# Optimization experiments

Hardware: AMD Instinct MI355X
Metric: run time of the kernel (lower is better)

The kernel has to match this reference:

```python
import jax, jax.numpy as jnp
import numpy as np
from jax import lax

T, H, I, E, K = 1024, 1024, 512, 16, 4


def setup_inputs() -> dict:
    key = jax.random.key(0)
    k1, k2, k3, k4, k5 = jax.random.split(key, 5)
    hidden_states = jax.random.normal(k1, (T, H), dtype=jnp.float32)
    top_k_index = jax.random.randint(k2, (T, K), 0, E)
    top_k_weights = jax.random.uniform(k3, (T, K), dtype=jnp.float32)
    gate_up_proj = jax.random.normal(k4, (E, 2 * I, H), dtype=jnp.float32) * 0.02
    down_proj = jax.random.normal(k5, (E, H, I), dtype=jnp.float32) * 0.02
    return {
        "hidden_states": hidden_states,
        "top_k_index": top_k_index,
        "top_k_weights": top_k_weights,
        "gate_up_proj": gate_up_proj,
        "down_proj": down_proj,
    }


def reference(hidden_states, top_k_index, top_k_weights, gate_up_proj, down_proj):
    num_experts = gate_up_proj.shape[0]
    # combine[t, e] = sum_k top_k_weights[t, k] * [top_k_index[t, k] == e]
    # Expert output is linear in the routing weight, so summing weights over
    # duplicate (token, expert) hits matches the original index_add_ exactly.
    one_hot = jax.nn.one_hot(top_k_index, num_experts, dtype=hidden_states.dtype)  # [T, K, E]
    combine = jnp.einsum("tke,tk->te", one_hot, top_k_weights)  # [T, E]

    def expert_step(acc, xs):
        w_gu, w_d, c = xs  # [2I, H], [H, I], [T]
        gu = hidden_states @ w_gu.T          # [T, 2I]
        gate, up = jnp.split(gu, 2, axis=-1)
        h = jax.nn.silu(gate) * up            # [T, I]
        out = h @ w_d.T                       # [T, H]
        return acc + out * c[:, None], None

    final, _ = lax.scan(
        expert_step,
        jnp.zeros_like(hidden_states),
        (gate_up_proj, down_proj, combine.T),
    )
    return final
```

## Files before the change

kernel.cpp:

```cpp
#include <hip/hip_runtime.h>
#include <hip/hip_bf16.h>
#include <cstdint>
#include <cstddef>

#define T_TOK 1024
#define HDIM  1024
#define IDIM  512
#define NEXP  16
#define TOPK  4
#define CAP   1024

typedef __bf16 bf16;
typedef __attribute__((ext_vector_type(8))) __bf16 bf16x8;
typedef __attribute__((ext_vector_type(4))) __bf16 bf16x4;
typedef __attribute__((ext_vector_type(4))) float f32x4;

__device__ __forceinline__ void lds_load16(void* lds_dst, const void* g_src) {
  __builtin_amdgcn_global_load_lds(
      (__attribute__((address_space(1))) unsigned int*)(void*)(g_src),
      (__attribute__((address_space(3))) unsigned int*)(lds_dst),
      16, 0, 0);
}

__device__ __forceinline__ bf16x4 cvt4(float4 a) {
  bf16x4 o;
  o[0] = (bf16)a.x; o[1] = (bf16)a.y; o[2] = (bf16)a.z; o[3] = (bf16)a.w;
  return o;
}


#define CVT_BLOCKS (T_TOK * HDIM / 4 / 256)

__global__ void prep_kernel(const float* __restrict__ hid_f, bf16* __restrict__ hid_b,
                            const int* __restrict__ idx, const float* __restrict__ w,
                            int* __restrict__ etk, float* __restrict__ ew,
                            int* __restrict__ cntpad, float* __restrict__ out) {
  __shared__ int cnt;
  const int b = blockIdx.x;
  const int tid = threadIdx.x;
  if (b < CVT_BLOCKS) {
    int i = b * 256 + tid;
    float4 v = ((const float4*)hid_f)[i];
    ((bf16x4*)hid_b)[i] = cvt4(v);
    ((float4*)out)[i] = make_float4(0.f, 0.f, 0.f, 0.f);
    if (b == 0)
      ((bf16x4*)(hid_b + (size_t)T_TOK * HDIM))[tid] = cvt4(make_float4(0.f, 0.f, 0.f, 0.f));
    return;
  }
  const int e = b - CVT_BLOCKS;
  if (tid == 0) cnt = 0;
  __syncthreads();
  for (int j = tid; j < T_TOK * TOPK; j += blockDim.x) {
    if (idx[j] == e) {
      int slot = atomicAdd(&cnt, 1);
      if (slot < CAP) { etk[e * CAP + slot] = j; ew[e * CAP + slot] = w[j]; }
    }
  }
  __syncthreads();
  int c = cnt < CAP ? cnt : CAP;
  int p = (c + 127) & ~127;
  for (int j = c + tid; j < p; j += blockDim.x) {
    etk[e * CAP + j] = (T_TOK << 2);
    ew[e * CAP + j] = 0.f;
  }
  if (tid == 0) cntpad[e] = p;
}


__global__ __launch_bounds__(256, 4) void gemm1_kernel(
    const bf16* __restrict__ hid,
    const float* __restrict__ gup,
    const int* __restrict__ etk, const float* __restrict__ ew,
    const int* __restrict__ cntpad,
    bf16* __restrict__ hsc) {
  __shared__ __align__(16) bf16 As[2][128 * 64];
  __shared__ __align__(16) bf16 Bs[2][32 * 64];
  const int e = blockIdx.y;
  const int ntiles = cntpad[e] >> 7;
  const int n0 = blockIdx.x * 16;
  const int ebase = e * CAP;
  const int tid = threadIdx.x, lane = tid & 63, wid = tid >> 6;
  const int wm = wid * 32;
  const int lcol = lane & 15, lquad = lane >> 4;
  const int l7 = lcol & 7;
  const int srow = tid >> 3;
  const int swz = ((tid & 7) ^ (srow & 7)) * 8;
  const int r = tid >> 3;
  const int c0 = (tid & 7) * 8;
  const int grow = (r < 16) ? (n0 + r) : (IDIM + n0 + (r - 16));
  const float* gB = gup + (size_t)e * (2 * IDIM) * HDIM + (size_t)grow * HDIM + c0;
  int wb[2];
#pragma unroll
  for (int j = 0; j < 2; ++j) {
    int c = c0 + 4 * j;
    wb[j] = (((c >> 3) ^ (r & 7)) * 8) + (c & 7);
  }
  const int bst = r * 64;

  for (int mt = 0; mt < ntiles; ++mt) {
    const int mrow = ebase + mt * 128;
    const bf16* gA[4];
#pragma unroll
    for (int q = 0; q < 4; ++q)
      gA[q] = hid + (size_t)(etk[mrow + srow + 32 * q] >> 2) * HDIM + swz;
    f32x4 aG[2], aU[2];
#pragma unroll
    for (int mf = 0; mf < 2; ++mf) {
      aG[mf] = f32x4{0.f, 0.f, 0.f, 0.f};
      aU[mf] = f32x4{0.f, 0.f, 0.f, 0.f};
    }
    {
      float4 bv[2];
#pragma unroll
      for (int j = 0; j < 2; ++j) bv[j] = *(const float4*)(gB + 4 * j);
#pragma unroll
      for (int q = 0; q < 4; ++q)
        lds_load16(&As[0][tid * 8 + q * 2048], gA[q]);
#pragma unroll
      for (int j = 0; j < 2; ++j)
        *(bf16x4*)&Bs[0][bst + wb[j]] = cvt4(bv[j]);
    }
    __syncthreads();
#pragma unroll 2
    for (int k = 0; k < 16; ++k) {
      const int cur = k & 1, nxt = cur ^ 1;
      float4 bn[2];
      if (k < 15) {
#pragma unroll
        for (int q = 0; q < 4; ++q)
          lds_load16(&As[nxt][tid * 8 + q * 2048], gA[q] + (k + 1) * 64);
#pragma unroll
        for (int j = 0; j < 2; ++j)
          bn[j] = *(const float4*)(gB + (k + 1) * 64 + 4 * j);
      }
      __builtin_amdgcn_s_setprio(1);
#pragma unroll
      for (int ks = 0; ks < 2; ++ks) {
        const int lch = ks * 4 + lquad;
        const int sw = (lch ^ l7) * 8;
        bf16x8 bg = *(const bf16x8*)&Bs[cur][lcol * 64 + sw];
        bf16x8 bu = *(const bf16x8*)&Bs[cur][(16 + lcol) * 64 + sw];
#pragma unroll
        for (int mf = 0; mf < 2; ++mf) {
          bf16x8 af = *(const bf16x8*)&As[cur][(wm + mf * 16 + lcol) * 64 + sw];
          aG[mf] = __builtin_amdgcn_mfma_f32_16x16x32_bf16(af, bg, aG[mf], 0, 0, 0);
          aU[mf] = __builtin_amdgcn_mfma_f32_16x16x32_bf16(af, bu, aU[mf], 0, 0, 0);
        }
      }
      __builtin_amdgcn_s_setprio(0);
      if (k < 15) {
#pragma unroll
        for (int j = 0; j < 2; ++j)
          *(bf16x4*)&Bs[nxt][bst + wb[j]] = cvt4(bn[j]);
      }
      __syncthreads();
    }
#pragma unroll
    for (int mf = 0; mf < 2; ++mf) {
#pragma unroll
      for (int rr = 0; rr < 4; ++rr) {
        const int erow = mt * 128 + wm + mf * 16 + lquad * 4 + rr;
        const float wgt = ew[ebase + erow];
        float g = aG[mf][rr], u = aU[mf][rr];
        float s = g / (1.f + __expf(-g));
        hsc[(size_t)(ebase + erow) * IDIM + n0 + lcol] = (bf16)(s * u * wgt);
      }
    }
  }
}


__global__ __launch_bounds__(256, 4) void gemm2_kernel(
    const bf16* __restrict__ hsc,
    const float* __restrict__ down,
    const int* __restrict__ etk, const int* __restrict__ cntpad,
    float* __restrict__ out) {
  __shared__ __align__(16) bf16 As[2][128 * 64];
  __shared__ __align__(16) bf16 Bs[2][32 * 64];
  const int flat = blockIdx.y * 32 + blockIdx.x;
  const int wkid = (flat & 7) * 64 + (flat >> 3);
  const int e = wkid >> 5;
  const int n0 = (wkid & 31) * 32;
  const int ntiles = cntpad[e] >> 7;
  const int ebase = e * CAP;
  const int tid = threadIdx.x, lane = tid & 63, wid = tid >> 6;
  const int wm = wid * 32;
  const int lcol = lane & 15, lquad = lane >> 4;
  const int l7 = lcol & 7;
  const int srow = tid >> 3;
  const int swz = ((tid & 7) ^ (srow & 7)) * 8;
  const int r = tid >> 3;
  const int c0 = (tid & 7) * 8;
  const float* gB = down + (size_t)e * HDIM * IDIM + (size_t)(n0 + r) * IDIM + c0;
  int wb[2];
#pragma unroll
  for (int j = 0; j < 2; ++j) {
    int c = c0 + 4 * j;
    wb[j] = (((c >> 3) ^ (r & 7)) * 8) + (c & 7);
  }
  const int bst = r * 64;

  for (int mt = 0; mt < ntiles; ++mt) {
    const size_t rbase = (size_t)(ebase + mt * 128);
    const bf16* gA[4];
#pragma unroll
    for (int q = 0; q < 4; ++q)
      gA[q] = hsc + (rbase + srow + 32 * q) * IDIM + swz;
    f32x4 acc[2][2];
#pragma unroll
    for (int mf = 0; mf < 2; ++mf) {
      acc[mf][0] = f32x4{0.f, 0.f, 0.f, 0.f};
      acc[mf][1] = f32x4{0.f, 0.f, 0.f, 0.f};
    }
    {
      float4 bv[2];
#pragma unroll
      for (int j = 0; j < 2; ++j) bv[j] = *(const float4*)(gB + 4 * j);
#pragma unroll
      for (int q = 0; q < 4; ++q)
        lds_load16(&As[0][tid * 8 + q * 2048], gA[q]);
#pragma unroll
      for (int j = 0; j < 2; ++j)
        *(bf16x4*)&Bs[0][bst + wb[j]] = cvt4(bv[j]);
    }
    __syncthreads();
#pragma unroll 2
    for (int k = 0; k < 8; ++k) {
      const int cur = k & 1, nxt = cur ^ 1;
      float4 bn[2];
      if (k < 7) {
#pragma unroll
        for (int q = 0; q < 4; ++q)
          lds_load16(&As[nxt][tid * 8 + q * 2048], gA[q] + (k + 1) * 64);
#pragma unroll
        for (int j = 0; j < 2; ++j)
          bn[j] = *(const float4*)(gB + (k + 1) * 64 + 4 * j);
      }
      __builtin_amdgcn_s_setprio(1);
#pragma unroll
      for (int ks = 0; ks < 2; ++ks) {
        const int lch = ks * 4 + lquad;
        const int sw = (lch ^ l7) * 8;
        bf16x8 b0 = *(const bf16x8*)&Bs[cur][lcol * 64 + sw];
        bf16x8 b1 = *(const bf16x8*)&Bs[cur][(16 + lcol) * 64 + sw];
#pragma unroll
        for (int mf = 0; mf < 2; ++mf) {
          bf16x8 af = *(const bf16x8*)&As[cur][(wm + mf * 16 + lcol) * 64 + sw];
          acc[mf][0] = __builtin_amdgcn_mfma_f32_16x16x32_bf16(af, b0, acc[mf][0], 0, 0, 0);
          acc[mf][1] = __builtin_amdgcn_mfma_f32_16x16x32_bf16(af, b1, acc[mf][1], 0, 0, 0);
        }
      }
      __builtin_amdgcn_s_setprio(0);
      if (k < 7) {
#pragma unroll
        for (int j = 0; j < 2; ++j)
          *(bf16x4*)&Bs[nxt][bst + wb[j]] = cvt4(bn[j]);
      }
      __syncthreads();
    }
#pragma unroll
    for (int mf = 0; mf < 2; ++mf) {
#pragma unroll
      for (int rr = 0; rr < 4; ++rr) {
        const int row = mt * 128 + wm + mf * 16 + lquad * 4 + rr;
        const int tk = etk[ebase + row];
        const int tok = tk >> 2;
        if (tok < T_TOK) {
          float* orow = out + (size_t)tok * HDIM + n0 + lcol;
          atomicAdd(orow, acc[mf][0][rr]);
          atomicAdd(orow + 16, acc[mf][1][rr]);
        }
      }
    }
  }
}


extern "C" void kernel_launch(void* const* d_in, const int* in_sizes, int n_in,
                              void* d_out, int out_size, void* d_ws, size_t ws_size,
                              hipStream_t stream) {
  const float* hid_f  = (const float*)d_in[0];
  const int*   idx    = (const int*)d_in[1];
  const float* tw     = (const float*)d_in[2];
  const float* gup_f  = (const float*)d_in[3];
  const float* down_f = (const float*)d_in[4];
  float* out = (float*)d_out;

  uint8_t* ws = (uint8_t*)d_ws;
  size_t off = 0;
  bf16* hid_b = (bf16*)(ws + off);   off += (size_t)(T_TOK + 1) * HDIM * 2;
  int*  etk   = (int*)(ws + off);    off += (size_t)NEXP * CAP * 4;
  float* ewt  = (float*)(ws + off);  off += (size_t)NEXP * CAP * 4;
  int* cntpad = (int*)(ws + off);    off += 256;
  bf16* hsc   = (bf16*)(ws + off);

  prep_kernel<<<dim3(CVT_BLOCKS + NEXP), dim3(256), 0, stream>>>(
      hid_f, hid_b, idx, tw, etk, ewt, cntpad, out);
  gemm1_kernel<<<dim3(IDIM / 16, NEXP, 1), dim3(256), 0, stream>>>(
      hid_b, gup_f, etk, ewt, cntpad, hsc);
  gemm2_kernel<<<dim3(HDIM / 32, NEXP, 1), dim3(256), 0, stream>>>(
      hsc, down_f, etk, cntpad, out);
}
```

Before: 209.6 us.

## Flatten expert GEMMs into per-tile grids with 64-row tiles and per-wave B

Both GEMM kernels stop looping over an expert's row tiles inside one block. Instead they launch a flattened grid of (expert, 64-row tile) entries, with a lookup over the padded per-expert counts; padding granularity drops from 128 to 64. Each wave now converts and stages its own private fp32→bf16 weight slice in LDS, and the next slice is prefetched in registers. The goal is more blocks in flight and better load balance across uneven expert loads. The cost is redundant tile-lookup work, blocks that exit early beyond the real tile count, and a larger register footprint for the prefetch buffers.

```diff
diff --git a/kernel.cpp b/kernel.cpp
--- a/kernel.cpp
+++ b/kernel.cpp
@@ -9,11 +9,15 @@
 #define NEXP  16
 #define TOPK  4
 #define CAP   1024
+#define MAXTILES 80
 
 typedef __bf16 bf16;
 typedef __attribute__((ext_vector_type(8))) __bf16 bf16x8;
 typedef __attribute__((ext_vector_type(4))) __bf16 bf16x4;
 typedef __attribute__((ext_vector_type(4))) float f32x4;
+
+#define BAR() __builtin_amdgcn_s_barrier()
+#define SB()  __builtin_amdgcn_sched_barrier(0)
 
 __device__ __forceinline__ void lds_load16(void* lds_dst, const void* g_src) {
   __builtin_amdgcn_global_load_lds(
@@ -26,6 +30,17 @@
   bf16x4 o;
   o[0] = (bf16)a.x; o[1] = (bf16)a.y; o[2] = (bf16)a.z; o[3] = (bf16)a.w;
   return o;
+}
+
+__device__ __forceinline__ bool tile_lookup(const int* cntpad, int idx,
+                                            int& e_out, int& mt_out) {
+  int rem = idx;
+  for (int e = 0; e < NEXP; ++e) {
+    int nt = cntpad[e] >> 6;
+    if (rem < nt) { e_out = e; mt_out = rem; return true; }
+    rem -= nt;
+  }
+  return false;
 }
 
 
@@ -58,7 +73,7 @@
   }
   __syncthreads();
   int c = cnt < CAP ? cnt : CAP;
-  int p = (c + 127) & ~127;
+  int p = (c + 63) & ~63;
   for (int j = c + tid; j < p; j += blockDim.x) {
     etk[e * CAP + j] = (T_TOK << 2);
     ew[e * CAP + j] = 0.f;
@@ -73,98 +88,102 @@
     const int* __restrict__ etk, const float* __restrict__ ew,
     const int* __restrict__ cntpad,
     bf16* __restrict__ hsc) {
-  __shared__ __align__(16) bf16 As[2][128 * 64];
-  __shared__ __align__(16) bf16 Bs[2][32 * 64];
-  const int e = blockIdx.y;
-  const int ntiles = cntpad[e] >> 7;
-  const int n0 = blockIdx.x * 16;
+  __shared__ __align__(16) bf16 As[2][64 * 64];
+  __shared__ __align__(16) bf16 Bp[4][32 * 64];
+  int e, mt;
+  if (!tile_lookup(cntpad, blockIdx.y, e, mt)) return;
+  const int n0 = blockIdx.x * 32;
   const int ebase = e * CAP;
   const int tid = threadIdx.x, lane = tid & 63, wid = tid >> 6;
-  const int wm = wid * 32;
+  const int wm = (wid >> 1) * 32, wi = (wid & 1) * 16;
   const int lcol = lane & 15, lquad = lane >> 4;
   const int l7 = lcol & 7;
   const int srow = tid >> 3;
   const int swz = ((tid & 7) ^ (srow & 7)) * 8;
-  const int r = tid >> 3;
-  const int c0 = (tid & 7) * 8;
-  const int grow = (r < 16) ? (n0 + r) : (IDIM + n0 + (r - 16));
-  const float* gB = gup + (size_t)e * (2 * IDIM) * HDIM + (size_t)grow * HDIM + c0;
-  int wb[2];
-#pragma unroll
-  for (int j = 0; j < 2; ++j) {
-    int c = c0 + 4 * j;
-    wb[j] = (((c >> 3) ^ (r & 7)) * 8) + (c & 7);
-  }
-  const int bst = r * 64;
-
-  for (int mt = 0; mt < ntiles; ++mt) {
-    const int mrow = ebase + mt * 128;
-    const bf16* gA[4];
-#pragma unroll
-    for (int q = 0; q < 4; ++q)
-      gA[q] = hid + (size_t)(etk[mrow + srow + 32 * q] >> 2) * HDIM + swz;
-    f32x4 aG[2], aU[2];
-#pragma unroll
-    for (int mf = 0; mf < 2; ++mf) {
-      aG[mf] = f32x4{0.f, 0.f, 0.f, 0.f};
-      aU[mf] = f32x4{0.f, 0.f, 0.f, 0.f};
-    }
-    {
-      float4 bv[2];
-#pragma unroll
-      for (int j = 0; j < 2; ++j) bv[j] = *(const float4*)(gB + 4 * j);
-#pragma unroll
-      for (int q = 0; q < 4; ++q)
-        lds_load16(&As[0][tid * 8 + q * 2048], gA[q]);
-#pragma unroll
-      for (int j = 0; j < 2; ++j)
-        *(bf16x4*)&Bs[0][bst + wb[j]] = cvt4(bv[j]);
-    }
-    __syncthreads();
-#pragma unroll 2
-    for (int k = 0; k < 16; ++k) {
-      const int cur = k & 1, nxt = cur ^ 1;
-      float4 bn[2];
-      if (k < 15) {
-#pragma unroll
-        for (int q = 0; q < 4; ++q)
-          lds_load16(&As[nxt][tid * 8 + q * 2048], gA[q] + (k + 1) * 64);
-#pragma unroll
-        for (int j = 0; j < 2; ++j)
-          bn[j] = *(const float4*)(gB + (k + 1) * 64 + 4 * j);
-      }
-      __builtin_amdgcn_s_setprio(1);
-#pragma unroll
-      for (int ks = 0; ks < 2; ++ks) {
-        const int lch = ks * 4 + lquad;
-        const int sw = (lch ^ l7) * 8;
-        bf16x8 bg = *(const bf16x8*)&Bs[cur][lcol * 64 + sw];
-        bf16x8 bu = *(const bf16x8*)&Bs[cur][(16 + lcol) * 64 + sw];
-#pragma unroll
-        for (int mf = 0; mf < 2; ++mf) {
-          bf16x8 af = *(const bf16x8*)&As[cur][(wm + mf * 16 + lcol) * 64 + sw];
-          aG[mf] = __builtin_amdgcn_mfma_f32_16x16x32_bf16(af, bg, aG[mf], 0, 0, 0);
-          aU[mf] = __builtin_amdgcn_mfma_f32_16x16x32_bf16(af, bu, aU[mf], 0, 0, 0);
-        }
-      }
-      __builtin_amdgcn_s_setprio(0);
-      if (k < 15) {
-#pragma unroll
-        for (int j = 0; j < 2; ++j)
-          *(bf16x4*)&Bs[nxt][bst + wb[j]] = cvt4(bn[j]);
-      }
-      __syncthreads();
-    }
-#pragma unroll
-    for (int mf = 0; mf < 2; ++mf) {
-#pragma unroll
-      for (int rr = 0; rr < 4; ++rr) {
-        const int erow = mt * 128 + wm + mf * 16 + lquad * 4 + rr;
-        const float wgt = ew[ebase + erow];
-        float g = aG[mf][rr], u = aU[mf][rr];
-        float s = g / (1.f + __expf(-g));
-        hsc[(size_t)(ebase + erow) * IDIM + n0 + lcol] = (bf16)(s * u * wgt);
-      }
+  const bf16* gA[2];
+#pragma unroll
+  for (int q = 0; q < 2; ++q)
+    gA[q] = hid + (size_t)(etk[ebase + mt * 64 + srow + 32 * q] >> 2) * HDIM + swz;
+  const int br = lane >> 2, bc = (lane & 3) * 4;
+  const float* gG = gup + (size_t)e * (2 * IDIM) * HDIM
+                  + (size_t)(n0 + wi + br) * HDIM + bc;
+  const float* gU = gG + (size_t)IDIM * HDIM;
+  bf16* myB = &Bp[wid][0];
+  int wG[4], wU[4];
+#pragma unroll
+  for (int j = 0; j < 4; ++j) {
+    int cf = bc + j * 16;
+    int s = (((cf >> 3) ^ (br & 7)) * 8) + (cf & 7);
+    wG[j] = br * 64 + s;
+    wU[j] = (16 + br) * 64 + s;
+  }
+
+  f32x4 aG[2], aU[2];
+#pragma unroll
+  for (int mf = 0; mf < 2; ++mf) {
+    aG[mf] = f32x4{0.f, 0.f, 0.f, 0.f};
+    aU[mf] = f32x4{0.f, 0.f, 0.f, 0.f};
+  }
+  float4 gA_[2][4], uA_[2][4];
+
+#pragma unroll
+  for (int q = 0; q < 2; ++q)
+    lds_load16(&As[0][tid * 8 + q * 2048], gA[q]);
+#pragma unroll
+  for (int j = 0; j < 4; ++j) {
+    gA_[0][j] = *(const float4*)(gG + j * 16);
+    uA_[0][j] = *(const float4*)(gU + j * 16);
+  }
+
+#pragma unroll
+  for (int k = 0; k < 16; ++k) {
+    const int cur = k & 1, nxt = cur ^ 1;
+    const int cs = k & 1;
+    const int ns = cs ^ 1;
+#pragma unroll
+    for (int j = 0; j < 4; ++j) {
+      *(bf16x4*)&myB[wG[j]] = cvt4(gA_[cs][j]);
+      *(bf16x4*)&myB[wU[j]] = cvt4(uA_[cs][j]);
+    }
+    SB();
+    BAR();
+    SB();
+    if (k + 1 < 16) {
+#pragma unroll
+      for (int q = 0; q < 2; ++q)
+        lds_load16(&As[nxt][tid * 8 + q * 2048], gA[q] + (k + 1) * 64);
+#pragma unroll
+      for (int j = 0; j < 4; ++j) {
+        gA_[ns][j] = *(const float4*)(gG + (k + 1) * 64 + j * 16);
+        uA_[ns][j] = *(const float4*)(gU + (k + 1) * 64 + j * 16);
+      }
+    }
+    __builtin_amdgcn_s_setprio(1);
+#pragma unroll
+    for (int ks = 0; ks < 2; ++ks) {
+      const int sw = ((ks * 4 + lquad) ^ l7) * 8;
+      bf16x8 bg = *(const bf16x8*)&myB[lcol * 64 + sw];
+      bf16x8 bu = *(const bf16x8*)&myB[(16 + lcol) * 64 + sw];
+#pragma unroll
+      for (int mf = 0; mf < 2; ++mf) {
+        const int row = wm + mf * 16 + lcol;
+        bf16x8 af = *(const bf16x8*)&As[cur][row * 64 + ((ks * 4 + lquad) ^ (row & 7)) * 8];
+        aG[mf] = __builtin_amdgcn_mfma_f32_16x16x32_bf16(af, bg, aG[mf], 0, 0, 0);
+        aU[mf] = __builtin_amdgcn_mfma_f32_16x16x32_bf16(af, bu, aU[mf], 0, 0, 0);
+      }
+    }
+    __builtin_amdgcn_s_setprio(0);
+  }
+
+#pragma unroll
+  for (int mf = 0; mf < 2; ++mf) {
+#pragma unroll
+    for (int rr = 0; rr < 4; ++rr) {
+      const int erow = mt * 64 + wm + mf * 16 + lquad * 4 + rr;
+      const float wgt = ew[ebase + erow];
+      float g = aG[mf][rr], u = aU[mf][rr];
+      float s = g / (1.f + __expf(-g));
+      hsc[(size_t)(ebase + erow) * IDIM + n0 + wi + lcol] = (bf16)(s * u * wgt);
     }
   }
 }
@@ -175,101 +194,104 @@
     const float* __restrict__ down,
     const int* __restrict__ etk, const int* __restrict__ cntpad,
     float* __restrict__ out) {
-  __shared__ __align__(16) bf16 As[2][128 * 64];
-  __shared__ __align__(16) bf16 Bs[2][32 * 64];
-  const int flat = blockIdx.y * 32 + blockIdx.x;
-  const int wkid = (flat & 7) * 64 + (flat >> 3);
-  const int e = wkid >> 5;
-  const int n0 = (wkid & 31) * 32;
-  const int ntiles = cntpad[e] >> 7;
+  __shared__ __align__(16) bf16 As[2][64 * 64];
+  __shared__ __align__(16) bf16 Bp[4][32 * 64];
+  int e, mt;
+  if (!tile_lookup(cntpad, blockIdx.y, e, mt)) return;
+  const int n0 = blockIdx.x * 64;
   const int ebase = e * CAP;
   const int tid = threadIdx.x, lane = tid & 63, wid = tid >> 6;
-  const int wm = wid * 32;
+  const int wm = (wid >> 1) * 32, wh = (wid & 1) * 32;
   const int lcol = lane & 15, lquad = lane >> 4;
   const int l7 = lcol & 7;
   const int srow = tid >> 3;
   const int swz = ((tid & 7) ^ (srow & 7)) * 8;
-  const int r = tid >> 3;
-  const int c0 = (tid & 7) * 8;
-  const float* gB = down + (size_t)e * HDIM * IDIM + (size_t)(n0 + r) * IDIM + c0;
-  int wb[2];
-#pragma unroll
-  for (int j = 0; j < 2; ++j) {
-    int c = c0 + 4 * j;
-    wb[j] = (((c >> 3) ^ (r & 7)) * 8) + (c & 7);
-  }
-  const int bst = r * 64;
-
-  for (int mt = 0; mt < ntiles; ++mt) {
-    const size_t rbase = (size_t)(ebase + mt * 128);
-    const bf16* gA[4];
-#pragma unroll
-    for (int q = 0; q < 4; ++q)
-      gA[q] = hsc + (rbase + srow + 32 * q) * IDIM + swz;
-    f32x4 acc[2][2];
-#pragma unroll
-    for (int mf = 0; mf < 2; ++mf) {
-      acc[mf][0] = f32x4{0.f, 0.f, 0.f, 0.f};
-      acc[mf][1] = f32x4{0.f, 0.f, 0.f, 0.f};
-    }
-    {
-      float4 bv[2];
-#pragma unroll
-      for (int j = 0; j < 2; ++j) bv[j] = *(const float4*)(gB + 4 * j);
-#pragma unroll
-      for (int q = 0; q < 4; ++q)
-        lds_load16(&As[0][tid * 8 + q * 2048], gA[q]);
-#pragma unroll
-      for (int j = 0; j < 2; ++j)
-        *(bf16x4*)&Bs[0][bst + wb[j]] = cvt4(bv[j]);
-    }
-    __syncthreads();
-#pragma unroll 2
-    for (int k = 0; k < 8; ++k) {
-      const int cur = k & 1, nxt = cur ^ 1;
-      float4 bn[2];
-      if (k < 7) {
-#pragma unroll
-        for (int q = 0; q < 4; ++q)
-          lds_load16(&As[nxt][tid * 8 + q * 2048], gA[q] + (k + 1) * 64);
-#pragma unroll
-        for (int j = 0; j < 2; ++j)
-          bn[j] = *(const float4*)(gB + (k + 1) * 64 + 4 * j);
-      }
-      __builtin_amdgcn_s_setprio(1);
-#pragma unroll
-      for (int ks = 0; ks < 2; ++ks) {
-        const int lch = ks * 4 + lquad;
-        const int sw = (lch ^ l7) * 8;
-        bf16x8 b0 = *(const bf16x8*)&Bs[cur][lcol * 64 + sw];
-        bf16x8 b1 = *(const bf16x8*)&Bs[cur][(16 + lcol) * 64 + sw];
-#pragma unroll
-        for (int mf = 0; mf < 2; ++mf) {
-          bf16x8 af = *(const bf16x8*)&As[cur][(wm + mf * 16 + lcol) * 64 + sw];
-          acc[mf][0] = __builtin_amdgcn_mfma_f32_16x16x32_bf16(af, b0, acc[mf][0], 0, 0, 0);
-          acc[mf][1] = __builtin_amdgcn_mfma_f32_16x16x32_bf16(af, b1, acc[mf][1], 0, 0, 0);
-        }
-      }
-      __builtin_amdgcn_s_setprio(0);
-      if (k < 7) {
-#pragma unroll
-        for (int j = 0; j < 2; ++j)
-          *(bf16x4*)&Bs[nxt][bst + wb[j]] = cvt4(bn[j]);
-      }
-      __syncthreads();
-    }
-#pragma unroll
-    for (int mf = 0; mf < 2; ++mf) {
-#pragma unroll
-      for (int rr = 0; rr < 4; ++rr) {
-        const int row = mt * 128 + wm + mf * 16 + lquad * 4 + rr;
-        const int tk = etk[ebase + row];
-        const int tok = tk >> 2;
-        if (tok < T_TOK) {
-          float* orow = out + (size_t)tok * HDIM + n0 + lcol;
-          atomicAdd(orow, acc[mf][0][rr]);
-          atomicAdd(orow + 16, acc[mf][1][rr]);
-        }
+  const bf16* gA[2];
+#pragma unroll
+  for (int q = 0; q < 2; ++q)
+    gA[q] = hsc + (size_t)(ebase + mt * 64 + srow + 32 * q) * IDIM + swz;
+  const int br = lane >> 2, bc = (lane & 3) * 4;
+  const float* gB = down + (size_t)e * HDIM * IDIM
+                  + (size_t)(n0 + wh + br) * IDIM + bc;
+  const float* gB1 = gB + (size_t)16 * IDIM;
+  bf16* myB = &Bp[wid][0];
+  int wB[2][4];
+#pragma unroll
+  for (int p = 0; p < 2; ++p)
+#pragma unroll
+    for (int j = 0; j < 4; ++j) {
+      int cf = bc + j * 16;
+      int s = (((cf >> 3) ^ (br & 7)) * 8) + (cf & 7);
+      wB[p][j] = (p * 16 + br) * 64 + s;
+    }
+
+  f32x4 acc[2][2];
+#pragma unroll
+  for (int mf = 0; mf < 2; ++mf) {
+    acc[mf][0] = f32x4{0.f, 0.f, 0.f, 0.f};
+    acc[mf][1] = f32x4{0.f, 0.f, 0.f, 0.f};
+  }
+  float4 b0_[2][4], b1_[2][4];
+
+#pragma unroll
+  for (int q = 0; q < 2; ++q)
+    lds_load16(&As[0][tid * 8 + q * 2048], gA[q]);
+#pragma unroll
+  for (int j = 0; j < 4; ++j) {
+    b0_[0][j] = *(const float4*)(gB + j * 16);
+    b1_[0][j] = *(const float4*)(gB1 + j * 16);
+  }
+
+#pragma unroll
+  for (int k = 0; k < 8; ++k) {
+    const int cur = k & 1, nxt = cur ^ 1;
+    const int cs = k & 1, ns = cs ^ 1;
+#pragma unroll
+    for (int j = 0; j < 4; ++j) {
+      *(bf16x4*)&myB[wB[0][j]] = cvt4(b0_[cs][j]);
+      *(bf16x4*)&myB[wB[1][j]] = cvt4(b1_[cs][j]);
+    }
+    SB();
+    BAR();
+    SB();
+    if (k + 1 < 8) {
+#pragma unroll
+      for (int q = 0; q < 2; ++q)
+        lds_load16(&As[nxt][tid * 8 + q * 2048], gA[q] + (k + 1) * 64);
+#pragma unroll
+      for (int j = 0; j < 4; ++j) {
+        b0_[ns][j] = *(const float4*)(gB + (k + 1) * 64 + j * 16);
+        b1_[ns][j] = *(const float4*)(gB1 + (k + 1) * 64 + j * 16);
+      }
+    }
+    __builtin_amdgcn_s_setprio(1);
+#pragma unroll
+    for (int ks = 0; ks < 2; ++ks) {
+      const int sw = ((ks * 4 + lquad) ^ l7) * 8;
+      bf16x8 bf0 = *(const bf16x8*)&myB[lcol * 64 + sw];
+      bf16x8 bf1 = *(const bf16x8*)&myB[(16 + lcol) * 64 + sw];
+#pragma unroll
+      for (int mf = 0; mf < 2; ++mf) {
+        const int row = wm + mf * 16 + lcol;
+        bf16x8 af = *(const bf16x8*)&As[cur][row * 64 + ((ks * 4 + lquad) ^ (row & 7)) * 8];
+        acc[mf][0] = __builtin_amdgcn_mfma_f32_16x16x32_bf16(af, bf0, acc[mf][0], 0, 0, 0);
+        acc[mf][1] = __builtin_amdgcn_mfma_f32_16x16x32_bf16(af, bf1, acc[mf][1], 0, 0, 0);
+      }
+    }
+    __builtin_amdgcn_s_setprio(0);
+  }
+
+#pragma unroll
+  for (int mf = 0; mf < 2; ++mf) {
+#pragma unroll
+    for (int rr = 0; rr < 4; ++rr) {
+      const int row = mt * 64 + wm + mf * 16 + lquad * 4 + rr;
+      const int tk = etk[ebase + row];
+      const int tok = tk >> 2;
+      if (tok < T_TOK) {
+        float* orow = out + (size_t)tok * HDIM + n0 + wh + lcol;
+        atomicAdd(orow, acc[mf][0][rr]);
+        atomicAdd(orow + 16, acc[mf][1][rr]);
       }
     }
   }
@@ -296,8 +318,8 @@
 
   prep_kernel<<<dim3(CVT_BLOCKS + NEXP), dim3(256), 0, stream>>>(
       hid_f, hid_b, idx, tw, etk, ewt, cntpad, out);
-  gemm1_kernel<<<dim3(IDIM / 16, NEXP, 1), dim3(256), 0, stream>>>(
+  gemm1_kernel<<<dim3(IDIM / 32, MAXTILES), dim3(256), 0, stream>>>(
       hid_b, gup_f, etk, ewt, cntpad, hsc);
-  gemm2_kernel<<<dim3(HDIM / 32, NEXP, 1), dim3(256), 0, stream>>>(
+  gemm2_kernel<<<dim3(HDIM / 64, MAXTILES), dim3(256), 0, stream>>>(
       hsc, down_f, etk, cntpad, out);
 }
```

Result: no change. 209.2 us (-0.2%).
